# Optimization experiments

Hardware: AMD Instinct MI355X
Metric: run time of the kernel (lower is better)

## Reference

```python
import jax, jax.numpy as jnp
import numpy as np
import math

D_MODEL = 1024
N_HEAD = 16
D_HEAD = D_MODEL // N_HEAD


def setup_inputs() -> dict:
    key = jax.random.key(0)
    k0, k1, k2, k3, k4 = jax.random.split(key, 5)
    B, N = 4, 2048
    inp = jax.random.normal(k0, (B, N, D_MODEL), dtype=jnp.float32)
    # causal mask: True = keep (masked_fill on ~mask)
    mask = jnp.tril(jnp.ones((N, N), dtype=bool))
    # qkv_proj Linear(d_model, 3*d_model); output Linear(d_model, d_model)
    s_in = 1.0 / math.sqrt(D_MODEL)
    W_qkv = jax.random.uniform(k1, (D_MODEL, 3 * D_MODEL), jnp.float32, -s_in, s_in)
    b_qkv = jax.random.uniform(k2, (3 * D_MODEL,), jnp.float32, -s_in, s_in)
    W_out = jax.random.uniform(k3, (D_MODEL, D_MODEL), jnp.float32, -s_in, s_in)
    b_out = jax.random.uniform(k4, (D_MODEL,), jnp.float32, -s_in, s_in)
    return {"input": inp, "W_qkv": W_qkv, "b_qkv": b_qkv,
            "W_out": W_out, "b_out": b_out, "mask": mask}


def reference(input, W_qkv, b_qkv, W_out, b_out, mask):
    B, N, d = input.shape
    qkv = input @ W_qkv + b_qkv                       # [B,N,3d]  (dropout=eval no-op)
    q, k, v = jnp.split(qkv, 3, axis=-1)
    # [B,N,H,Dh] -> [B,H,N,Dh]
    q = q.reshape(B, N, N_HEAD, D_HEAD).transpose(0, 2, 1, 3)
    k = k.reshape(B, N, N_HEAD, D_HEAD).transpose(0, 2, 1, 3)
    v = v.reshape(B, N, N_HEAD, D_HEAD).transpose(0, 2, 1, 3)
    scale = 1.0 / math.sqrt(D_HEAD)
    scores = jnp.einsum('bhqd,bhkd->bhqk', q, k) * scale   # [B,H,N,N]
    scores = jnp.where(mask, scores, -jnp.inf)
    attn = jax.nn.softmax(scores, axis=-1)
    out = jnp.einsum('bhqk,bhkd->bhqd', attn, v)           # [B,H,N,Dh]
    out = out.transpose(0, 2, 1, 3).reshape(B, N, d)       # concat heads
    return out @ W_out + b_out
```

## Files before the change

### kernel.cpp

```cpp
#include <hip/hip_runtime.h>
#include <hip/hip_bf16.h>

typedef unsigned short u16;
typedef unsigned u32;
typedef __attribute__((ext_vector_type(4))) unsigned short u16x4;
typedef __attribute__((ext_vector_type(8))) unsigned short u16x8;
typedef __attribute__((ext_vector_type(4))) unsigned u32x4;
typedef __attribute__((ext_vector_type(8))) __bf16 bf16x8;
typedef __attribute__((ext_vector_type(4))) float f32x4;

typedef __attribute__((address_space(1))) void as1v;
typedef __attribute__((address_space(3))) void as3v;

#define MFMA16(a, b, c) __builtin_amdgcn_mfma_f32_16x16x32_bf16(a, b, c, 0, 0, 0)

#if __has_builtin(__builtin_amdgcn_permlane16_swap) && __has_builtin(__builtin_amdgcn_permlane32_swap)
#define HAVE_PERMLANE_SWAP 1
#else
#define HAVE_PERMLANE_SWAP 0
#endif

__device__ __forceinline__ u16 f2bf(float f) {
    unsigned u = __builtin_bit_cast(unsigned, f);
    u += 0x7fffu + ((u >> 16) & 1u);
    return (u16)(u >> 16);
}

__device__ __forceinline__ u32 pkbf(float lo, float hi) {
    u32 r;
    asm("v_cvt_pk_bf16_f32 %0, %1, %2" : "=v"(r) : "v"(lo), "v"(hi));
    return r;
}

__device__ __forceinline__ void gload16(const void* g, void* l) {
    __builtin_amdgcn_global_load_lds((as1v*)g, (as3v*)l, 16, 0, 0);
}

__device__ __forceinline__ float redmax_cross(float v) {
#if HAVE_PERMLANE_SWAP
    u32 xu = __builtin_bit_cast(u32, v);
    auto r16 = __builtin_amdgcn_permlane16_swap(xu, xu, false, false);
    float a = fmaxf(__builtin_bit_cast(float, (u32)r16[0]),
                    __builtin_bit_cast(float, (u32)r16[1]));
    u32 au = __builtin_bit_cast(u32, a);
    auto r32 = __builtin_amdgcn_permlane32_swap(au, au, false, false);
    return fmaxf(__builtin_bit_cast(float, (u32)r32[0]),
                 __builtin_bit_cast(float, (u32)r32[1]));
#else
    v = fmaxf(v, __shfl_xor(v, 16, 64));
    return fmaxf(v, __shfl_xor(v, 32, 64));
#endif
}

__device__ __forceinline__ float redsum_cross(float v) {
#if HAVE_PERMLANE_SWAP
    u32 xu = __builtin_bit_cast(u32, v);
    auto r16 = __builtin_amdgcn_permlane16_swap(xu, xu, false, false);
    float a = __builtin_bit_cast(float, (u32)r16[0]) +
              __builtin_bit_cast(float, (u32)r16[1]);
    u32 au = __builtin_bit_cast(u32, a);
    auto r32 = __builtin_amdgcn_permlane32_swap(au, au, false, false);
    return __builtin_bit_cast(float, (u32)r32[0]) +
           __builtin_bit_cast(float, (u32)r32[1]);
#else
    v += __shfl_xor(v, 16, 64);
    return v + __shfl_xor(v, 32, 64);
#endif
}

__global__ void convert_f32_bf16(const float* __restrict__ in, u16* __restrict__ out, int n4) {
    int i = blockIdx.x * blockDim.x + threadIdx.x;
    if (i < n4) {
        float4 v = *(const float4*)&in[(size_t)i * 4];
        u16x4 o;
        o.x = f2bf(v.x); o.y = f2bf(v.y); o.z = f2bf(v.z); o.w = f2bf(v.w);
        *(u16x4*)&out[(size_t)i * 4] = o;
    }
}

__global__ void transpose_convert(const float* __restrict__ in, u16* __restrict__ out, int R, int C) {
    __shared__ float tl[64][65];
    const int rb = blockIdx.x, cb = blockIdx.y;
    const int tid = threadIdx.x;
    for (int it = 0; it < 4; ++it) {
        int lin = (tid + it * 256) * 4;
        int r = lin >> 6, c = lin & 63;
        float4 v = *(const float4*)&in[(size_t)(rb * 64 + r) * C + cb * 64 + c];
        tl[r][c + 0] = v.x; tl[r][c + 1] = v.y; tl[r][c + 2] = v.z; tl[r][c + 3] = v.w;
    }
    __syncthreads();
    for (int it = 0; it < 4; ++it) {
        int lin = (tid + it * 256) * 4;
        int oc = lin >> 6, orr = lin & 63;
        u16x4 o;
        o.x = f2bf(tl[orr + 0][oc]);
        o.y = f2bf(tl[orr + 1][oc]);
        o.z = f2bf(tl[orr + 2][oc]);
        o.w = f2bf(tl[orr + 3][oc]);
        *(u16x4*)&out[(size_t)(cb * 64 + oc) * R + rb * 64 + orr] = o;
    }
}

__global__ __launch_bounds__(256, 3) void gemm128_qkv(
    const u16* __restrict__ A, const u16* __restrict__ Bt, const float* __restrict__ bias,
    u16* __restrict__ qb, u16* __restrict__ kb, u16* __restrict__ vtb) {
    constexpr int K = 1024;
    constexpr int NT = 32;
    __shared__ u16 ldsu[24576];

    const int bid = blockIdx.x;
    const int s = (bid & 7) * 192 + (bid >> 3);
    const int bm = s / 24, bn = s % 24;

    const int tid = threadIdx.x, wid = tid >> 6, lane = tid & 63;
    const int wr = wid >> 1, wc = wid & 1;
    const int l15 = lane & 15, lhi = lane >> 4;

    const int sslot = (lane & 7) ^ (lane >> 3);
    const int kcol = (sslot & 3) * 8;
    const int mloc = (lane >> 3) * 2 + (sslot >> 2);

    const u16* Arow[2];
    const u16* Brow[2];
#pragma unroll
    for (int li = 0; li < 2; ++li) {
        int sg = wid * 2 + li;
        Arow[li] = A + (size_t)(bm * 128 + sg * 16 + mloc) * K + kcol;
        Brow[li] = Bt + (size_t)(bn * 128 + sg * 16 + mloc) * K + kcol;
    }

    auto stageA = [&](int buf, int t) {
#pragma unroll
        for (int li = 0; li < 2; ++li) {
            int sg = wid * 2 + li;
            gload16(Arow[li] + t * 32, (char*)ldsu + buf * 16384 + sg * 1024);
        }
    };
    auto stageB = [&](int buf, int t) {
#pragma unroll
        for (int li = 0; li < 2; ++li) {
            int sg = wid * 2 + li;
            gload16(Brow[li] + t * 32, (char*)ldsu + buf * 16384 + 8192 + sg * 1024);
        }
    };

    const int rslot = ((l15 & 1) * 4 + lhi) ^ ((l15 >> 1) & 7);
    const int fragoff = (l15 >> 1) * 64 + rslot * 8;

    f32x4 acc[4][4];
#pragma unroll
    for (int i = 0; i < 4; ++i)
#pragma unroll
        for (int j = 0; j < 4; ++j) acc[i][j] = (f32x4){0.f, 0.f, 0.f, 0.f};

    auto doTile = [&](int cur, int tstage, bool dostage) {
        const u16* Ab = ldsu + cur * 8192 + wr * 2048 + fragoff;
        const u16* Bb = ldsu + cur * 8192 + 4096 + wc * 2048 + fragoff;
        bf16x8 af[4], b0, b1;
#pragma unroll
        for (int mf = 0; mf < 4; ++mf) af[mf] = *(const bf16x8*)(Ab + mf * 512);
        b0 = *(const bf16x8*)(Bb);
        b1 = *(const bf16x8*)(Bb + 512);
        if (dostage) stageA((tstage * 43691) >> 17  == -1 ? 0 : tstage % 3, tstage);
        __builtin_amdgcn_s_setprio(1);
#pragma unroll
        for (int mf = 0; mf < 4; ++mf) {
            acc[mf][0] = MFMA16(af[mf], b0, acc[mf][0]);
            acc[mf][1] = MFMA16(af[mf], b1, acc[mf][1]);
        }
        __builtin_amdgcn_s_setprio(0);
        b0 = *(const bf16x8*)(Bb + 1024);
        b1 = *(const bf16x8*)(Bb + 1536);
        if (dostage) stageB(tstage % 3, tstage);
        __builtin_amdgcn_s_setprio(1);
#pragma unroll
        for (int mf = 0; mf < 4; ++mf) {
            acc[mf][2] = MFMA16(af[mf], b0, acc[mf][2]);
            acc[mf][3] = MFMA16(af[mf], b1, acc[mf][3]);
        }
        __builtin_amdgcn_s_setprio(0);
    };

    stageA(0, 0); stageB(0, 0);
    stageA(1, 1); stageB(1, 1);
    asm volatile("s_waitcnt vmcnt(4)" ::: "memory");
    __builtin_amdgcn_s_barrier();
    __builtin_amdgcn_sched_barrier(0);

    for (int t = 0; t < NT - 2; ++t) {
        doTile(t % 3, t + 2, true);
        asm volatile("s_waitcnt vmcnt(4)" ::: "memory");
        __builtin_amdgcn_s_barrier();
        __builtin_amdgcn_sched_barrier(0);
    }
    doTile((NT - 2) % 3, 0, false);
    asm volatile("s_waitcnt vmcnt(0)" ::: "memory");
    __builtin_amdgcn_s_barrier();
    __builtin_amdgcn_sched_barrier(0);
    doTile((NT - 1) % 3, 0, false);

    const int cg0 = bn * 128 + wc * 64;
    const int which = cg0 >> 10, rem = cg0 & 1023;
    const int hh = rem >> 6, dh0 = rem & 63;
    const int rgb0 = bm * 128 + wr * 64;
    const int bb = rgb0 >> 11, n0 = rgb0 & 2047;

    if (which == 2) {
        const size_t vbase = ((size_t)(bb * 16 + hh) * 64 + dh0) * 2048 + (size_t)n0;
#pragma unroll
        for (int nt = 0; nt < 4; ++nt) {
            float bv = bias[cg0 + nt * 16 + l15];
            size_t rowb = vbase + (size_t)(nt * 16 + l15) * 2048;
#pragma unroll
            for (int mt = 0; mt < 4; ++mt) {
                u16x4 w;
#pragma unroll
                for (int v = 0; v < 4; ++v) w[v] = f2bf(acc[mt][nt][v] + bv);
                *(u16x4*)&vtb[rowb + mt * 16 + lhi * 4] = w;
            }
        }
    } else {
        u16* dst = (which == 0) ? qb : kb;
        const float qs = (which == 0) ? 0.18033688011112042f : 1.0f;
        const size_t gbase = (((size_t)bb * 16 + hh) * 2048 + n0) * 64 + dh0;
#pragma unroll
        for (int nt = 0; nt < 4; ++nt) {
            float bv = bias[cg0 + nt * 16 + l15];
#pragma unroll
            for (int mt = 0; mt < 4; ++mt)
#pragma unroll
                for (int v = 0; v < 4; ++v) {
                    int n = mt * 16 + lhi * 4 + v;
                    dst[gbase + (size_t)n * 64 + nt * 16 + l15] =
                        f2bf((acc[mt][nt][v] + bv) * qs);
                }
        }
    }
}

__global__ __launch_bounds__(512, 2) void gemm256_out(
    const u16* __restrict__ A, const u16* __restrict__ Bt, const float* __restrict__ bias,
    float* __restrict__ outf) {
    constexpr int K = 1024;
    constexpr int NT = 32;
    __shared__ u16 ldsu[49152];

    const int bid = blockIdx.x;
    const int swz = (bid & 7) * 32 + (bid >> 3);
    const int bm = swz >> 3, bn = swz & 7;

    const int tid = threadIdx.x, wid = tid >> 6, lane = tid & 63;
    const int wr = wid >> 2, wc = wid & 3;
    const int l15 = lane & 15, lhi = lane >> 4;

    const int sslot = (lane & 7) ^ (lane >> 3);
    const int kcol = (sslot & 3) * 8;
    const int mloc = (lane >> 3) * 2 + (sslot >> 2);

    const u16* Arow[2];
#pragma unroll
    for (int li = 0; li < 2; ++li) {
        int sg = wid * 2 + li;
        Arow[li] = A + (size_t)(bm * 256 + sg * 16 + mloc) * K + kcol;
    }
    const u16* Brow = Bt + (size_t)(bn * 128 + wid * 16 + mloc) * K + kcol;

    auto stageA = [&](int buf, int t) {
#pragma unroll
        for (int li = 0; li < 2; ++li) {
            int sg = wid * 2 + li;
            gload16(Arow[li] + t * 32, (char*)ldsu + buf * 24576 + sg * 1024);
        }
    };
    auto stageB = [&](int buf, int t) {
        gload16(Brow + t * 32, (char*)ldsu + buf * 24576 + 16384 + wid * 1024);
    };

    const int rslot = ((l15 & 1) * 4 + lhi) ^ ((l15 >> 1) & 7);
    const int fragoff = (l15 >> 1) * 64 + rslot * 8;

    f32x4 acc[8][2];
#pragma unroll
    for (int i = 0; i < 8; ++i) {
        acc[i][0] = (f32x4){0.f, 0.f, 0.f, 0.f};
        acc[i][1] = (f32x4){0.f, 0.f, 0.f, 0.f};
    }

    auto doTile = [&](int cur, int tstage, bool dostage) {
        const u16* Ab = ldsu + cur * 12288 + wr * 4096 + fragoff;
        const u16* Bb = ldsu + cur * 12288 + 8192 + wc * 1024 + fragoff;
        bf16x8 af[8], b0, b1;
#pragma unroll
        for (int mf = 0; mf < 8; ++mf) af[mf] = *(const bf16x8*)(Ab + mf * 512);
        b0 = *(const bf16x8*)(Bb);
        b1 = *(const bf16x8*)(Bb + 512);
        if (dostage) stageA(tstage & 3, tstage);
        __builtin_amdgcn_s_setprio(1);
#pragma unroll
        for (int mf = 0; mf < 8; ++mf) acc[mf][0] = MFMA16(af[mf], b0, acc[mf][0]);
        __builtin_amdgcn_s_setprio(0);
        if (dostage) stageB(tstage & 3, tstage);
        __builtin_amdgcn_s_setprio(1);
#pragma unroll
        for (int mf = 0; mf < 8; ++mf) acc[mf][1] = MFMA16(af[mf], b1, acc[mf][1]);
        __builtin_amdgcn_s_setprio(0);
    };

    stageA(0, 0); stageB(0, 0);
    stageA(1, 1); stageB(1, 1);
    stageA(2, 2); stageB(2, 2);
    asm volatile("s_waitcnt vmcnt(6)" ::: "memory");
    __builtin_amdgcn_s_barrier();
    __builtin_amdgcn_sched_barrier(0);

    for (int t = 0; t < NT - 3; ++t) {
        doTile(t & 3, t + 3, true);
        asm volatile("s_waitcnt vmcnt(6)" ::: "memory");
        __builtin_amdgcn_s_barrier();
        __builtin_amdgcn_sched_barrier(0);
    }
    doTile((NT - 3) & 3, 0, false);
    asm volatile("s_waitcnt vmcnt(3)" ::: "memory");
    __builtin_amdgcn_s_barrier();
    __builtin_amdgcn_sched_barrier(0);
    doTile((NT - 2) & 3, 0, false);
    asm volatile("s_waitcnt vmcnt(0)" ::: "memory");
    __builtin_amdgcn_s_barrier();
    __builtin_amdgcn_sched_barrier(0);
    doTile((NT - 1) & 3, 0, false);

#pragma unroll
    for (int nf = 0; nf < 2; ++nf) {
        int cg = bn * 128 + wc * 32 + nf * 16 + l15;
        float bv = bias[cg];
#pragma unroll
        for (int mf = 0; mf < 8; ++mf) {
            int rgb = bm * 256 + wr * 128 + mf * 16 + lhi * 4;
#pragma unroll
            for (int v = 0; v < 4; ++v)
                outf[(size_t)(rgb + v) * 1024 + cg] = acc[mf][nf][v] + bv;
        }
    }
}

__global__ __launch_bounds__(256, 4) void attn_kernel(
    const u16* __restrict__ qbuf, const u16* __restrict__ kbuf,
    const u16* __restrict__ vtb, u16* __restrict__ obuf) {
    __shared__ u16 Kl[2][64 * 64];
    __shared__ u16 Vl[2][64 * 64];
    const int bid = blockIdx.x;
    const int rr = bid >> 8;
    const int pp = (bid >> 6) & 3;
    const int c = (rr & 1) ? (((rr >> 1) << 2) + pp)
                           : (15 - ((rr >> 1) << 2) - pp);
    const int bh = ((bid & 7) << 3) + ((bid >> 3) & 7);
    const int b = bh >> 4, h = bh & 15;
    const int tid = threadIdx.x, wid = tid >> 6, lane = tid & 63;
    const int l15 = lane & 15, lhi = lane >> 4;
    const int q0 = c * 128 + wid * 32;
    const int ntW = 2 * c + (wid >> 1) + 1;
    const int ntmax = 2 * c + 2;

    auto loadQ = [&](int qbase, bf16x8* dst) {
        const u16* qp = qbuf + ((size_t)bh * 2048 + qbase + l15) * 64 + lhi * 8;
        dst[0] = *(const bf16x8*)(qp);
        dst[1] = *(const bf16x8*)(qp + 32);
    };
    bf16x8 qf0[2], qf1[2];
    loadQ(q0, qf0); loadQ(q0 + 16, qf1);

    float m0 = -1e30f, l0 = 0.f, m1 = -1e30f, l1 = 0.f;
    f32x4 o0[4], o1[4];
#pragma unroll
    for (int d = 0; d < 4; ++d) {
        o0[d] = (f32x4){0.f, 0.f, 0.f, 0.f};
        o1[d] = (f32x4){0.f, 0.f, 0.f, 0.f};
    }

    const int srow = lane >> 3;
    const int scolb = ((lane & 7) * 16) ^ (srow << 4);

    auto stage = [&](int buf, int t) {
        const int kbase = t * 64;
#pragma unroll
        for (int s = 0; s < 2; ++s) {
            int sg = wid * 2 + s;
            int row = sg * 8 + srow;
            const u16* gk = kbuf + ((size_t)bh * 2048 + kbase + row) * 64 + (scolb >> 1);
            gload16(gk, (char*)Kl[buf] + sg * 1024);
            const u16* gv = vtb + ((size_t)bh * 64 + row) * 2048 + kbase + (scolb >> 1);
            gload16(gv, (char*)Vl[buf] + sg * 1024);
        }
    };

    auto smax = [&](f32x4* s, int qg0, int t, float& m, float& l, f32x4* oa, u32* pw) {
        const int qg = qg0 + l15;
        if (64 * t + 63 > qg0) {
#pragma unroll
            for (int kb4 = 0; kb4 < 4; ++kb4)
#pragma unroll
                for (int v = 0; v < 4; ++v) {
                    int kg = 64 * t + kb4 * 16 + lhi * 4 + v;
                    if (kg > qg) s[kb4][v] = -1e30f;
                }
        }
        float pm = fmaxf(fmaxf(fmaxf(s[0][0], s[0][1]), fmaxf(s[0][2], s[0][3])),
                         fmaxf(fmaxf(s[1][0], s[1][1]), fmaxf(s[1][2], s[1][3])));
        pm = fmaxf(pm, fmaxf(fmaxf(fmaxf(s[2][0], s[2][1]), fmaxf(s[2][2], s[2][3])),
                             fmaxf(fmaxf(s[3][0], s[3][1]), fmaxf(s[3][2], s[3][3]))));
        pm = redmax_cross(pm);
        if (!__all(pm <= m + 8.f)) {
            float nm = fmaxf(m, pm);
            float f = exp2f(m - nm);
            m = nm;
            l *= f;
#pragma unroll
            for (int d = 0; d < 4; ++d)
#pragma unroll
                for (int v = 0; v < 4; ++v) oa[d][v] *= f;
        }
        float rs = 0.f;
#pragma unroll
        for (int kb4 = 0; kb4 < 4; ++kb4)
#pragma unroll
            for (int v = 0; v < 4; ++v) {
                float e = exp2f(s[kb4][v] - m);
                s[kb4][v] = e;
                rs += e;
            }
        l += redsum_cross(rs);
        pw[0] = pkbf(s[0][0], s[0][1]); pw[1] = pkbf(s[0][2], s[0][3]);
        pw[2] = pkbf(s[1][0], s[1][1]); pw[3] = pkbf(s[1][2], s[1][3]);
        pw[4] = pkbf(s[2][0], s[2][1]); pw[5] = pkbf(s[2][2], s[2][3]);
        pw[6] = pkbf(s[3][0], s[3][1]); pw[7] = pkbf(s[3][2], s[3][3]);
    };

    auto computeChunk = [&](const char* Kb, const char* Vb, int t) {
        f32x4 s0[4], s1[4];
        __builtin_amdgcn_s_setprio(1);
#pragma unroll
        for (int kb4 = 0; kb4 < 4; ++kb4) {
            const int r = kb4 * 16 + l15;
            const int sw = (r & 7) << 4;
            const int rowb = r * 128;
            bf16x8 kf0 = *(const bf16x8*)(Kb + rowb + ((lhi * 16) ^ sw));
            bf16x8 kf1 = *(const bf16x8*)(Kb + rowb + ((64 + lhi * 16) ^ sw));
            f32x4 a0 = (f32x4){0.f, 0.f, 0.f, 0.f};
            a0 = MFMA16(kf0, qf0[0], a0);
            a0 = MFMA16(kf1, qf0[1], a0);
            s0[kb4] = a0;
            f32x4 a1 = (f32x4){0.f, 0.f, 0.f, 0.f};
            a1 = MFMA16(kf0, qf1[0], a1);
            a1 = MFMA16(kf1, qf1[1], a1);
            s1[kb4] = a1;
        }
        __builtin_amdgcn_s_setprio(0);
        u32 pw0[8], pw1[8];
        smax(s0, q0, t, m0, l0, o0, pw0);
        smax(s1, q0 + 16, t, m1, l1, o1, pw1);
        __builtin_amdgcn_s_setprio(1);
#pragma unroll
        for (int ks = 0; ks < 2; ++ks) {
            bf16x8 pb0 = __builtin_bit_cast(bf16x8,
                (u32x4){pw0[ks * 4 + 0], pw0[ks * 4 + 1], pw0[ks * 4 + 2], pw0[ks * 4 + 3]});
            bf16x8 pb1 = __builtin_bit_cast(bf16x8,
                (u32x4){pw1[ks * 4 + 0], pw1[ks * 4 + 1], pw1[ks * 4 + 2], pw1[ks * 4 + 3]});
#pragma unroll
            for (int dhb = 0; dhb < 4; ++dhb) {
                const int r = dhb * 16 + l15;
                const int sw = (r & 7) << 4;
                u16x4 v0 = *(const u16x4*)(Vb + r * 128 + ((ks * 64 + 8 * lhi) ^ sw));
                u16x4 v1 = *(const u16x4*)(Vb + r * 128 + ((ks * 64 + 32 + 8 * lhi) ^ sw));
                u16x8 vv = {v0[0], v0[1], v0[2], v0[3], v1[0], v1[1], v1[2], v1[3]};
                bf16x8 vf = __builtin_bit_cast(bf16x8, vv);
                o0[dhb] = MFMA16(vf, pb0, o0[dhb]);
                o1[dhb] = MFMA16(vf, pb1, o1[dhb]);
            }
        }
        __builtin_amdgcn_s_setprio(0);
    };

    stage(0, 0);
    int t = 0;
    for (;;) {
        __syncthreads();
        if (t + 1 < ntmax) stage(1, t + 1);
        if (t < ntW) computeChunk((const char*)Kl[0], (const char*)Vl[0], t);
        if (++t == ntmax) break;
        __syncthreads();
        if (t + 1 < ntmax) stage(0, t + 1);
        if (t < ntW) computeChunk((const char*)Kl[1], (const char*)Vl[1], t);
        if (++t == ntmax) break;
    }

    auto epi = [&](int qg0, float l, const f32x4* oa) {
        const float rl = 1.f / l;
        const int q = qg0 + l15;
        const size_t rowoff = ((size_t)b * 2048 + q) * 1024 + h * 64;
#pragma unroll
        for (int dhb = 0; dhb < 4; ++dhb) {
            u16x4 w;
#pragma unroll
            for (int v = 0; v < 4; ++v) w[v] = f2bf(oa[dhb][v] * rl);
            *(u16x4*)&obuf[rowoff + dhb * 16 + lhi * 4] = w;
        }
    };
    epi(q0, l0, o0);
    epi(q0 + 16, l1, o1);
}

extern "C" void kernel_launch(void* const* d_in, const int* in_sizes, int n_in,
                              void* d_out, int out_size, void* d_ws, size_t ws_size,
                              hipStream_t stream) {
    const float* inp   = (const float*)d_in[0];
    const float* W_qkv = (const float*)d_in[1];
    const float* b_qkv = (const float*)d_in[2];
    const float* W_out = (const float*)d_in[3];
    const float* b_out = (const float*)d_in[4];
    float* out = (float*)d_out;

    u16* xb   = (u16*)d_ws;
    u16* wqt  = xb + 8388608;
    u16* wot  = wqt + 3145728;
    u16* qbuf = wot + 1048576;
    u16* kbuf = qbuf + 8388608;
    u16* vtb  = kbuf + 8388608;
    u16* obuf = vtb + 8388608;

    convert_f32_bf16<<<8192, 256, 0, stream>>>(inp, xb, 2097152);
    transpose_convert<<<dim3(16, 48), 256, 0, stream>>>(W_qkv, wqt, 1024, 3072);
    transpose_convert<<<dim3(16, 16), 256, 0, stream>>>(W_out, wot, 1024, 1024);
    gemm128_qkv<<<1536, 256, 0, stream>>>(xb, wqt, b_qkv, qbuf, kbuf, vtb);
    attn_kernel<<<1024, 256, 0, stream>>>(qbuf, kbuf, vtb, obuf);
    gemm256_out<<<256, 512, 0, stream>>>(obuf, wot, b_out, out);
}
```

Baseline: 178.2 us.

## Split causal attention rows across blocks with log-sum-exp merge for balance

Each block pair now handles query chunk p fully plus half the key range of chunk 15-p, while the partner block does the other half. Partial outputs and their max/sum statistics are written out, and a new merge kernel combines them with log-sum-exp rescaling. The goal is equal work per block under the causal mask, replacing the earlier interleaved block ordering. The cost is an extra kernel launch, fp32 partial-output traffic through reused workspace, and a bf16 round trip on one of the two partials. It also simplifies a no-op expression in the GEMM stage index.

Measured after the change: 214.1 us. 1.2x slower.

```diff
diff --git a/kernel.cpp b/kernel.cpp
--- a/kernel.cpp
+++ b/kernel.cpp
@@ -24,6 +24,11 @@
     unsigned u = __builtin_bit_cast(unsigned, f);
     u += 0x7fffu + ((u >> 16) & 1u);
     return (u16)(u >> 16);
+}
+
+__device__ __forceinline__ float bf2f(u16 v) {
+    u32 u = ((u32)v) << 16;
+    return __builtin_bit_cast(float, u);
 }
 
 __device__ __forceinline__ u32 pkbf(float lo, float hi) {
@@ -161,7 +166,7 @@
         for (int mf = 0; mf < 4; ++mf) af[mf] = *(const bf16x8*)(Ab + mf * 512);
         b0 = *(const bf16x8*)(Bb);
         b1 = *(const bf16x8*)(Bb + 512);
-        if (dostage) stageA((tstage * 43691) >> 17  == -1 ? 0 : tstage % 3, tstage);
+        if (dostage) stageA(tstage % 3, tstage);
         __builtin_amdgcn_s_setprio(1);
 #pragma unroll
         for (int mf = 0; mf < 4; ++mf) {
@@ -345,37 +350,17 @@
 
 __global__ __launch_bounds__(256, 4) void attn_kernel(
     const u16* __restrict__ qbuf, const u16* __restrict__ kbuf,
-    const u16* __restrict__ vtb, u16* __restrict__ obuf) {
+    const u16* __restrict__ vtb, u16* __restrict__ obuf,
+    float* __restrict__ pbufA, float* __restrict__ mlbuf) {
     __shared__ u16 Kl[2][64 * 64];
     __shared__ u16 Vl[2][64 * 64];
     const int bid = blockIdx.x;
-    const int rr = bid >> 8;
-    const int pp = (bid >> 6) & 3;
-    const int c = (rr & 1) ? (((rr >> 1) << 2) + pp)
-                           : (15 - ((rr >> 1) << 2) - pp);
-    const int bh = ((bid & 7) << 3) + ((bid >> 3) & 7);
+    const int half = bid & 1;
+    const int p = (bid >> 1) & 7;
+    const int bh = bid >> 4;
     const int b = bh >> 4, h = bh & 15;
     const int tid = threadIdx.x, wid = tid >> 6, lane = tid & 63;
     const int l15 = lane & 15, lhi = lane >> 4;
-    const int q0 = c * 128 + wid * 32;
-    const int ntW = 2 * c + (wid >> 1) + 1;
-    const int ntmax = 2 * c + 2;
-
-    auto loadQ = [&](int qbase, bf16x8* dst) {
-        const u16* qp = qbuf + ((size_t)bh * 2048 + qbase + l15) * 64 + lhi * 8;
-        dst[0] = *(const bf16x8*)(qp);
-        dst[1] = *(const bf16x8*)(qp + 32);
-    };
-    bf16x8 qf0[2], qf1[2];
-    loadQ(q0, qf0); loadQ(q0 + 16, qf1);
-
-    float m0 = -1e30f, l0 = 0.f, m1 = -1e30f, l1 = 0.f;
-    f32x4 o0[4], o1[4];
-#pragma unroll
-    for (int d = 0; d < 4; ++d) {
-        o0[d] = (f32x4){0.f, 0.f, 0.f, 0.f};
-        o1[d] = (f32x4){0.f, 0.f, 0.f, 0.f};
-    }
 
     const int srow = lane >> 3;
     const int scolb = ((lane & 7) * 16) ^ (srow << 4);
@@ -393,120 +378,205 @@
         }
     };
 
-    auto smax = [&](f32x4* s, int qg0, int t, float& m, float& l, f32x4* oa, u32* pw) {
-        const int qg = qg0 + l15;
-        if (64 * t + 63 > qg0) {
+    auto run_piece = [&](int c, int t0, int t1, int mode) {
+        const int q0 = c * 128 + wid * 32;
+        bf16x8 qf0[2], qf1[2];
+        {
+            const u16* qp0 = qbuf + ((size_t)bh * 2048 + q0 + l15) * 64 + lhi * 8;
+            const u16* qp1 = qbuf + ((size_t)bh * 2048 + q0 + 16 + l15) * 64 + lhi * 8;
+            qf0[0] = *(const bf16x8*)(qp0); qf0[1] = *(const bf16x8*)(qp0 + 32);
+            qf1[0] = *(const bf16x8*)(qp1); qf1[1] = *(const bf16x8*)(qp1 + 32);
+        }
+        float m0 = -1e30f, l0 = 0.f, m1 = -1e30f, l1 = 0.f;
+        f32x4 o0[4], o1[4];
+#pragma unroll
+        for (int d = 0; d < 4; ++d) {
+            o0[d] = (f32x4){0.f, 0.f, 0.f, 0.f};
+            o1[d] = (f32x4){0.f, 0.f, 0.f, 0.f};
+        }
+        const int ntW = 2 * c + (wid >> 1) + 1;
+
+        auto smax = [&](f32x4* s, int qg0, int t, float& m, float& l, f32x4* oa, u32* pw) {
+            const int qg = qg0 + l15;
+            if (64 * t + 63 > qg0) {
+#pragma unroll
+                for (int kb4 = 0; kb4 < 4; ++kb4)
+#pragma unroll
+                    for (int v = 0; v < 4; ++v) {
+                        int kg = 64 * t + kb4 * 16 + lhi * 4 + v;
+                        if (kg > qg) s[kb4][v] = -1e30f;
+                    }
+            }
+            float pm = fmaxf(fmaxf(fmaxf(s[0][0], s[0][1]), fmaxf(s[0][2], s[0][3])),
+                             fmaxf(fmaxf(s[1][0], s[1][1]), fmaxf(s[1][2], s[1][3])));
+            pm = fmaxf(pm, fmaxf(fmaxf(fmaxf(s[2][0], s[2][1]), fmaxf(s[2][2], s[2][3])),
+                                 fmaxf(fmaxf(s[3][0], s[3][1]), fmaxf(s[3][2], s[3][3]))));
+            pm = redmax_cross(pm);
+            if (!__all(pm <= m + 8.f)) {
+                float nm = fmaxf(m, pm);
+                float f = exp2f(m - nm);
+                m = nm;
+                l *= f;
+#pragma unroll
+                for (int d = 0; d < 4; ++d)
+#pragma unroll
+                    for (int v = 0; v < 4; ++v) oa[d][v] *= f;
+            }
+            float rs = 0.f;
 #pragma unroll
             for (int kb4 = 0; kb4 < 4; ++kb4)
 #pragma unroll
                 for (int v = 0; v < 4; ++v) {
-                    int kg = 64 * t + kb4 * 16 + lhi * 4 + v;
-                    if (kg > qg) s[kb4][v] = -1e30f;
+                    float e = exp2f(s[kb4][v] - m);
+                    s[kb4][v] = e;
+                    rs += e;
                 }
-        }
-        float pm = fmaxf(fmaxf(fmaxf(s[0][0], s[0][1]), fmaxf(s[0][2], s[0][3])),
-                         fmaxf(fmaxf(s[1][0], s[1][1]), fmaxf(s[1][2], s[1][3])));
-        pm = fmaxf(pm, fmaxf(fmaxf(fmaxf(s[2][0], s[2][1]), fmaxf(s[2][2], s[2][3])),
-                             fmaxf(fmaxf(s[3][0], s[3][1]), fmaxf(s[3][2], s[3][3]))));
-        pm = redmax_cross(pm);
-        if (!__all(pm <= m + 8.f)) {
-            float nm = fmaxf(m, pm);
-            float f = exp2f(m - nm);
-            m = nm;
-            l *= f;
-#pragma unroll
-            for (int d = 0; d < 4; ++d)
-#pragma unroll
-                for (int v = 0; v < 4; ++v) oa[d][v] *= f;
-        }
-        float rs = 0.f;
-#pragma unroll
-        for (int kb4 = 0; kb4 < 4; ++kb4)
-#pragma unroll
-            for (int v = 0; v < 4; ++v) {
-                float e = exp2f(s[kb4][v] - m);
-                s[kb4][v] = e;
-                rs += e;
+            l += redsum_cross(rs);
+            pw[0] = pkbf(s[0][0], s[0][1]); pw[1] = pkbf(s[0][2], s[0][3]);
+            pw[2] = pkbf(s[1][0], s[1][1]); pw[3] = pkbf(s[1][2], s[1][3]);
+            pw[4] = pkbf(s[2][0], s[2][1]); pw[5] = pkbf(s[2][2], s[2][3]);
+            pw[6] = pkbf(s[3][0], s[3][1]); pw[7] = pkbf(s[3][2], s[3][3]);
+        };
+
+        auto computeChunk = [&](const char* Kb, const char* Vb, int t) {
+            f32x4 s0[4], s1[4];
+            __builtin_amdgcn_s_setprio(1);
+#pragma unroll
+            for (int kb4 = 0; kb4 < 4; ++kb4) {
+                const int r = kb4 * 16 + l15;
+                const int sw = (r & 7) << 4;
+                const int rowb = r * 128;
+                bf16x8 kf0 = *(const bf16x8*)(Kb + rowb + ((lhi * 16) ^ sw));
+                bf16x8 kf1 = *(const bf16x8*)(Kb + rowb + ((64 + lhi * 16) ^ sw));
+                f32x4 a0 = (f32x4){0.f, 0.f, 0.f, 0.f};
+                a0 = MFMA16(kf0, qf0[0], a0);
+                a0 = MFMA16(kf1, qf0[1], a0);
+                s0[kb4] = a0;
+                f32x4 a1 = (f32x4){0.f, 0.f, 0.f, 0.f};
+                a1 = MFMA16(kf0, qf1[0], a1);
+                a1 = MFMA16(kf1, qf1[1], a1);
+                s1[kb4] = a1;
             }
-        l += redsum_cross(rs);
-        pw[0] = pkbf(s[0][0], s[0][1]); pw[1] = pkbf(s[0][2], s[0][3]);
-        pw[2] = pkbf(s[1][0], s[1][1]); pw[3] = pkbf(s[1][2], s[1][3]);
-        pw[4] = pkbf(s[2][0], s[2][1]); pw[5] = pkbf(s[2][2], s[2][3]);
-        pw[6] = pkbf(s[3][0], s[3][1]); pw[7] = pkbf(s[3][2], s[3][3]);
-    };
-
-    auto computeChunk = [&](const char* Kb, const char* Vb, int t) {
-        f32x4 s0[4], s1[4];
-        __builtin_amdgcn_s_setprio(1);
-#pragma unroll
-        for (int kb4 = 0; kb4 < 4; ++kb4) {
-            const int r = kb4 * 16 + l15;
-            const int sw = (r & 7) << 4;
-            const int rowb = r * 128;
-            bf16x8 kf0 = *(const bf16x8*)(Kb + rowb + ((lhi * 16) ^ sw));
-            bf16x8 kf1 = *(const bf16x8*)(Kb + rowb + ((64 + lhi * 16) ^ sw));
-            f32x4 a0 = (f32x4){0.f, 0.f, 0.f, 0.f};
-            a0 = MFMA16(kf0, qf0[0], a0);
-            a0 = MFMA16(kf1, qf0[1], a0);
-            s0[kb4] = a0;
-            f32x4 a1 = (f32x4){0.f, 0.f, 0.f, 0.f};
-            a1 = MFMA16(kf0, qf1[0], a1);
-            a1 = MFMA16(kf1, qf1[1], a1);
-            s1[kb4] = a1;
-        }
-        __builtin_amdgcn_s_setprio(0);
-        u32 pw0[8], pw1[8];
-        smax(s0, q0, t, m0, l0, o0, pw0);
-        smax(s1, q0 + 16, t, m1, l1, o1, pw1);
-        __builtin_amdgcn_s_setprio(1);
-#pragma unroll
-        for (int ks = 0; ks < 2; ++ks) {
-            bf16x8 pb0 = __builtin_bit_cast(bf16x8,
-                (u32x4){pw0[ks * 4 + 0], pw0[ks * 4 + 1], pw0[ks * 4 + 2], pw0[ks * 4 + 3]});
-            bf16x8 pb1 = __builtin_bit_cast(bf16x8,
-                (u32x4){pw1[ks * 4 + 0], pw1[ks * 4 + 1], pw1[ks * 4 + 2], pw1[ks * 4 + 3]});
-#pragma unroll
-            for (int dhb = 0; dhb < 4; ++dhb) {
-                const int r = dhb * 16 + l15;
-                const int sw = (r & 7) << 4;
-                u16x4 v0 = *(const u16x4*)(Vb + r * 128 + ((ks * 64 + 8 * lhi) ^ sw));
-                u16x4 v1 = *(const u16x4*)(Vb + r * 128 + ((ks * 64 + 32 + 8 * lhi) ^ sw));
-                u16x8 vv = {v0[0], v0[1], v0[2], v0[3], v1[0], v1[1], v1[2], v1[3]};
-                bf16x8 vf = __builtin_bit_cast(bf16x8, vv);
-                o0[dhb] = MFMA16(vf, pb0, o0[dhb]);
-                o1[dhb] = MFMA16(vf, pb1, o1[dhb]);
+            __builtin_amdgcn_s_setprio(0);
+            u32 pw0[8], pw1[8];
+            smax(s0, q0, t, m0, l0, o0, pw0);
+            smax(s1, q0 + 16, t, m1, l1, o1, pw1);
+            __builtin_amdgcn_s_setprio(1);
+#pragma unroll
+            for (int ks = 0; ks < 2; ++ks) {
+                bf16x8 pb0 = __builtin_bit_cast(bf16x8,
+                    (u32x4){pw0[ks * 4 + 0], pw0[ks * 4 + 1], pw0[ks * 4 + 2], pw0[ks * 4 + 3]});
+                bf16x8 pb1 = __builtin_bit_cast(bf16x8,
+                    (u32x4){pw1[ks * 4 + 0], pw1[ks * 4 + 1], pw1[ks * 4 + 2], pw1[ks * 4 + 3]});
+#pragma unroll
+                for (int dhb = 0; dhb < 4; ++dhb) {
+                    const int r = dhb * 16 + l15;
+                    const int sw = (r & 7) << 4;
+                    u16x4 v0 = *(const u16x4*)(Vb + r * 128 + ((ks * 64 + 8 * lhi) ^ sw));
+                    u16x4 v1 = *(const u16x4*)(Vb + r * 128 + ((ks * 64 + 32 + 8 * lhi) ^ sw));
+                    u16x8 vv = {v0[0], v0[1], v0[2], v0[3], v1[0], v1[1], v1[2], v1[3]};
+                    bf16x8 vf = __builtin_bit_cast(bf16x8, vv);
+                    o0[dhb] = MFMA16(vf, pb0, o0[dhb]);
+                    o1[dhb] = MFMA16(vf, pb1, o1[dhb]);
+                }
             }
-        }
-        __builtin_amdgcn_s_setprio(0);
-    };
-
-    stage(0, 0);
-    int t = 0;
-    for (;;) {
+            __builtin_amdgcn_s_setprio(0);
+        };
+
         __syncthreads();
-        if (t + 1 < ntmax) stage(1, t + 1);
-        if (t < ntW) computeChunk((const char*)Kl[0], (const char*)Vl[0], t);
-        if (++t == ntmax) break;
-        __syncthreads();
-        if (t + 1 < ntmax) stage(0, t + 1);
-        if (t < ntW) computeChunk((const char*)Kl[1], (const char*)Vl[1], t);
-        if (++t == ntmax) break;
-    }
-
-    auto epi = [&](int qg0, float l, const f32x4* oa) {
-        const float rl = 1.f / l;
-        const int q = qg0 + l15;
-        const size_t rowoff = ((size_t)b * 2048 + q) * 1024 + h * 64;
-#pragma unroll
-        for (int dhb = 0; dhb < 4; ++dhb) {
-            u16x4 w;
-#pragma unroll
-            for (int v = 0; v < 4; ++v) w[v] = f2bf(oa[dhb][v] * rl);
-            *(u16x4*)&obuf[rowoff + dhb * 16 + lhi * 4] = w;
-        }
-    };
-    epi(q0, l0, o0);
-    epi(q0 + 16, l1, o1);
+        stage(0, t0);
+        int t = t0;
+        for (;;) {
+            __syncthreads();
+            if (t + 1 < t1) stage(((t - t0) & 1) ^ 1, t + 1);
+            if (t < ntW) computeChunk((const char*)Kl[(t - t0) & 1],
+                                      (const char*)Vl[(t - t0) & 1], t);
+            if (++t == t1) break;
+        }
+
+        const int pi = 15 - c;
+        if (mode == 0) {
+            auto epi = [&](int goff, float l, const f32x4* oa) {
+                const float rl = 1.f / l;
+                const int q = q0 + goff + l15;
+                const size_t rowoff = ((size_t)b * 2048 + q) * 1024 + h * 64;
+#pragma unroll
+                for (int dhb = 0; dhb < 4; ++dhb) {
+                    u16x4 w;
+#pragma unroll
+                    for (int v = 0; v < 4; ++v) w[v] = f2bf(oa[dhb][v] * rl);
+                    *(u16x4*)&obuf[rowoff + dhb * 16 + lhi * 4] = w;
+                }
+            };
+            epi(0, l0, o0);
+            epi(16, l1, o1);
+        } else if (mode == 1) {
+            auto epi = [&](int goff, float m, float l, const f32x4* oa) {
+                const int ql = wid * 32 + goff + l15;
+                const size_t rowi = ((size_t)bh * 8 + pi) * 128 + ql;
+                float* prow = pbufA + rowi * 64;
+#pragma unroll
+                for (int dhb = 0; dhb < 4; ++dhb)
+                    *(f32x4*)&prow[dhb * 16 + lhi * 4] = oa[dhb];
+                if (lhi == 0) { mlbuf[rowi] = m; mlbuf[65536 + rowi] = l; }
+            };
+            epi(0, m0, l0, o0);
+            epi(16, m1, l1, o1);
+        } else {
+            auto epi = [&](int goff, float m, float l, const f32x4* oa) {
+                const float rl = 1.f / l;
+                const int q = q0 + goff + l15;
+                const size_t rowoff = ((size_t)b * 2048 + q) * 1024 + h * 64;
+#pragma unroll
+                for (int dhb = 0; dhb < 4; ++dhb) {
+                    u16x4 w;
+#pragma unroll
+                    for (int v = 0; v < 4; ++v) w[v] = f2bf(oa[dhb][v] * rl);
+                    *(u16x4*)&obuf[rowoff + dhb * 16 + lhi * 4] = w;
+                }
+                const int ql = wid * 32 + goff + l15;
+                const size_t rowi = ((size_t)bh * 8 + pi) * 128 + ql;
+                if (lhi == 0) { mlbuf[131072 + rowi] = m; mlbuf[196608 + rowi] = l; }
+            };
+            epi(0, m0, l0, o0);
+            epi(16, m1, l1, o1);
+        }
+    };
+
+    if (half == 0) {
+        run_piece(p, 0, 2 * p + 2, 0);
+        run_piece(15 - p, 0, 15 - 2 * p, 1);
+    } else {
+        run_piece(15 - p, 15 - 2 * p, 32 - 2 * p, 2);
+    }
+}
+
+__global__ __launch_bounds__(256) void merge_lse(
+    const float* __restrict__ pbufA, const float* __restrict__ mlbuf,
+    u16* __restrict__ obuf) {
+    const int gid = blockIdx.x * 256 + threadIdx.x;
+    const int rid = gid >> 2, seg = gid & 3;
+    const float m1 = mlbuf[rid], l1 = mlbuf[65536 + rid];
+    const float m2 = mlbuf[131072 + rid], l2 = mlbuf[196608 + rid];
+    const float M = fmaxf(m1, m2);
+    const float f1 = exp2f(m1 - M), f2 = exp2f(m2 - M);
+    const float rden = 1.f / (l1 * f1 + l2 * f2);
+    const float w2 = l2 * f2;
+    const int bh = rid >> 10, rem = rid & 1023, pp = rem >> 7, ql = rem & 127;
+    const int b = bh >> 4, h = bh & 15;
+    const int qg = (15 - pp) * 128 + ql;
+    u16* orow = obuf + ((size_t)b * 2048 + qg) * 1024 + h * 64 + seg * 16;
+    const float* prow = pbufA + (size_t)rid * 64 + seg * 16;
+#pragma unroll
+    for (int j = 0; j < 4; ++j) {
+        f32x4 o1 = *(const f32x4*)&prow[j * 4];
+        u16x4 o2 = *(const u16x4*)&orow[j * 4];
+        u16x4 w;
+#pragma unroll
+        for (int v = 0; v < 4; ++v)
+            w[v] = f2bf((o1[v] * f1 + bf2f(o2[v]) * w2) * rden);
+        *(u16x4*)&orow[j * 4] = w;
+    }
 }
 
 extern "C" void kernel_launch(void* const* d_in, const int* in_sizes, int n_in,
@@ -526,11 +596,14 @@
     u16* kbuf = qbuf + 8388608;
     u16* vtb  = kbuf + 8388608;
     u16* obuf = vtb + 8388608;
+    float* pbufA = (float*)xb;
+    float* mlbuf = (float*)wqt;
 
     convert_f32_bf16<<<8192, 256, 0, stream>>>(inp, xb, 2097152);
     transpose_convert<<<dim3(16, 48), 256, 0, stream>>>(W_qkv, wqt, 1024, 3072);
     transpose_convert<<<dim3(16, 16), 256, 0, stream>>>(W_out, wot, 1024, 1024);
     gemm128_qkv<<<1536, 256, 0, stream>>>(xb, wqt, b_qkv, qbuf, kbuf, vtb);
-    attn_kernel<<<1024, 256, 0, stream>>>(qbuf, kbuf, vtb, obuf);
+    attn_kernel<<<1024, 256, 0, stream>>>(qbuf, kbuf, vtb, obuf, pbufA, mlbuf);
+    merge_lse<<<1024, 256, 0, stream>>>(pbufA, mlbuf, obuf);
     gemm256_out<<<256, 512, 0, stream>>>(obuf, wot, b_out, out);
 }
```

## Replace 256x128 output GEMM with 128x128 tiles and triple-buffered pipeline

Applied to the files above, without the earlier changes.

The output projection GEMM moves from 256x128 tiles with 512 threads and a 4-stage buffer to 128x128 tiles with 256 threads and a 3-stage buffer, which doubles the grid to 512 blocks. This reuses the QKV GEMM's tile structure, so the kernel uses less LDS and can fit more blocks per CU, and more blocks spread across the CUs. In exchange each block gets less operand reuse and one fewer prefetch stage. A no-op expression in the QKV stageA buffer index is also simplified.

Result: no change. 179.2 us (median of 2 runs) (+0.6%).

```diff
diff --git a/kernel.cpp b/kernel.cpp
--- a/kernel.cpp
+++ b/kernel.cpp
@@ -161,7 +161,7 @@
         for (int mf = 0; mf < 4; ++mf) af[mf] = *(const bf16x8*)(Ab + mf * 512);
         b0 = *(const bf16x8*)(Bb);
         b1 = *(const bf16x8*)(Bb + 512);
-        if (dostage) stageA((tstage * 43691) >> 17  == -1 ? 0 : tstage % 3, tstage);
+        if (dostage) stageA(tstage % 3, tstage);
         __builtin_amdgcn_s_setprio(1);
 #pragma unroll
         for (int mf = 0; mf < 4; ++mf) {
@@ -238,19 +238,19 @@
     }
 }
 
-__global__ __launch_bounds__(512, 2) void gemm256_out(
+__global__ __launch_bounds__(256, 3) void gemm128_out(
     const u16* __restrict__ A, const u16* __restrict__ Bt, const float* __restrict__ bias,
     float* __restrict__ outf) {
     constexpr int K = 1024;
     constexpr int NT = 32;
-    __shared__ u16 ldsu[49152];
+    __shared__ u16 ldsu[24576];
 
     const int bid = blockIdx.x;
-    const int swz = (bid & 7) * 32 + (bid >> 3);
-    const int bm = swz >> 3, bn = swz & 7;
+    const int s = (bid & 7) * 64 + (bid >> 3);
+    const int bm = s >> 3, bn = s & 7;
 
     const int tid = threadIdx.x, wid = tid >> 6, lane = tid & 63;
-    const int wr = wid >> 2, wc = wid & 3;
+    const int wr = wid >> 1, wc = wid & 1;
     const int l15 = lane & 15, lhi = lane >> 4;
 
     const int sslot = (lane & 7) ^ (lane >> 3);
@@ -258,87 +258,94 @@
     const int mloc = (lane >> 3) * 2 + (sslot >> 2);
 
     const u16* Arow[2];
+    const u16* Brow[2];
 #pragma unroll
     for (int li = 0; li < 2; ++li) {
         int sg = wid * 2 + li;
-        Arow[li] = A + (size_t)(bm * 256 + sg * 16 + mloc) * K + kcol;
-    }
-    const u16* Brow = Bt + (size_t)(bn * 128 + wid * 16 + mloc) * K + kcol;
+        Arow[li] = A + (size_t)(bm * 128 + sg * 16 + mloc) * K + kcol;
+        Brow[li] = Bt + (size_t)(bn * 128 + sg * 16 + mloc) * K + kcol;
+    }
 
     auto stageA = [&](int buf, int t) {
 #pragma unroll
         for (int li = 0; li < 2; ++li) {
             int sg = wid * 2 + li;
-            gload16(Arow[li] + t * 32, (char*)ldsu + buf * 24576 + sg * 1024);
+            gload16(Arow[li] + t * 32, (char*)ldsu + buf * 16384 + sg * 1024);
         }
     };
     auto stageB = [&](int buf, int t) {
-        gload16(Brow + t * 32, (char*)ldsu + buf * 24576 + 16384 + wid * 1024);
+#pragma unroll
+        for (int li = 0; li < 2; ++li) {
+            int sg = wid * 2 + li;
+            gload16(Brow[li] + t * 32, (char*)ldsu + buf * 16384 + 8192 + sg * 1024);
+        }
     };
 
     const int rslot = ((l15 & 1) * 4 + lhi) ^ ((l15 >> 1) & 7);
     const int fragoff = (l15 >> 1) * 64 + rslot * 8;
 
-    f32x4 acc[8][2];
-#pragma unroll
-    for (int i = 0; i < 8; ++i) {
-        acc[i][0] = (f32x4){0.f, 0.f, 0.f, 0.f};
-        acc[i][1] = (f32x4){0.f, 0.f, 0.f, 0.f};
-    }
+    f32x4 acc[4][4];
+#pragma unroll
+    for (int i = 0; i < 4; ++i)
+#pragma unroll
+        for (int j = 0; j < 4; ++j) acc[i][j] = (f32x4){0.f, 0.f, 0.f, 0.f};
 
     auto doTile = [&](int cur, int tstage, bool dostage) {
-        const u16* Ab = ldsu + cur * 12288 + wr * 4096 + fragoff;
-        const u16* Bb = ldsu + cur * 12288 + 8192 + wc * 1024 + fragoff;
-        bf16x8 af[8], b0, b1;
-#pragma unroll
-        for (int mf = 0; mf < 8; ++mf) af[mf] = *(const bf16x8*)(Ab + mf * 512);
+        const u16* Ab = ldsu + cur * 8192 + wr * 2048 + fragoff;
+        const u16* Bb = ldsu + cur * 8192 + 4096 + wc * 2048 + fragoff;
+        bf16x8 af[4], b0, b1;
+#pragma unroll
+        for (int mf = 0; mf < 4; ++mf) af[mf] = *(const bf16x8*)(Ab + mf * 512);
         b0 = *(const bf16x8*)(Bb);
         b1 = *(const bf16x8*)(Bb + 512);
-        if (dostage) stageA(tstage & 3, tstage);
+        if (dostage) stageA(tstage % 3, tstage);
         __builtin_amdgcn_s_setprio(1);
 #pragma unroll
-        for (int mf = 0; mf < 8; ++mf) acc[mf][0] = MFMA16(af[mf], b0, acc[mf][0]);
+        for (int mf = 0; mf < 4; ++mf) {
+            acc[mf][0] = MFMA16(af[mf], b0, acc[mf][0]);
+            acc[mf][1] = MFMA16(af[mf], b1, acc[mf][1]);
+        }
         __builtin_amdgcn_s_setprio(0);
-        if (dostage) stageB(tstage & 3, tstage);
+        b0 = *(const bf16x8*)(Bb + 1024);
+        b1 = *(const bf16x8*)(Bb + 1536);
+        if (dostage) stageB(tstage % 3, tstage);
         __builtin_amdgcn_s_setprio(1);
 #pragma unroll
-        for (int mf = 0; mf < 8; ++mf) acc[mf][1] = MFMA16(af[mf], b1, acc[mf][1]);
+        for (int mf = 0; mf < 4; ++mf) {
+            acc[mf][2] = MFMA16(af[mf], b0, acc[mf][2]);
+            acc[mf][3] = MFMA16(af[mf], b1, acc[mf][3]);
+        }
         __builtin_amdgcn_s_setprio(0);
     };
 
     stageA(0, 0); stageB(0, 0);
     stageA(1, 1); stageB(1, 1);
-    stageA(2, 2); stageB(2, 2);
-    asm volatile("s_waitcnt vmcnt(6)" ::: "memory");
+    asm volatile("s_waitcnt vmcnt(4)" ::: "memory");
     __builtin_amdgcn_s_barrier();
     __builtin_amdgcn_sched_barrier(0);
 
-    for (int t = 0; t < NT - 3; ++t) {
-        doTile(t & 3, t + 3, true);
-        asm volatile("s_waitcnt vmcnt(6)" ::: "memory");
+    for (int t = 0; t < NT - 2; ++t) {
+        doTile(t % 3, t + 2, true);
+        asm volatile("s_waitcnt vmcnt(4)" ::: "memory");
         __builtin_amdgcn_s_barrier();
         __builtin_amdgcn_sched_barrier(0);
     }
-    doTile((NT - 3) & 3, 0, false);
-    asm volatile("s_waitcnt vmcnt(3)" ::: "memory");
-    __builtin_amdgcn_s_barrier();
-    __builtin_amdgcn_sched_barrier(0);
-    doTile((NT - 2) & 3, 0, false);
+    doTile((NT - 2) % 3, 0, false);
     asm volatile("s_waitcnt vmcnt(0)" ::: "memory");
     __builtin_amdgcn_s_barrier();
     __builtin_amdgcn_sched_barrier(0);
-    doTile((NT - 1) & 3, 0, false);
-
-#pragma unroll
-    for (int nf = 0; nf < 2; ++nf) {
-        int cg = bn * 128 + wc * 32 + nf * 16 + l15;
+    doTile((NT - 1) % 3, 0, false);
+
+#pragma unroll
+    for (int nt = 0; nt < 4; ++nt) {
+        int cg = bn * 128 + wc * 64 + nt * 16 + l15;
         float bv = bias[cg];
 #pragma unroll
-        for (int mf = 0; mf < 8; ++mf) {
-            int rgb = bm * 256 + wr * 128 + mf * 16 + lhi * 4;
+        for (int mt = 0; mt < 4; ++mt) {
+            int rg = bm * 128 + wr * 64 + mt * 16 + lhi * 4;
 #pragma unroll
             for (int v = 0; v < 4; ++v)
-                outf[(size_t)(rgb + v) * 1024 + cg] = acc[mf][nf][v] + bv;
+                outf[(size_t)(rg + v) * 1024 + cg] = acc[mt][nt][v] + bv;
         }
     }
 }
@@ -532,5 +539,5 @@
     transpose_convert<<<dim3(16, 16), 256, 0, stream>>>(W_out, wot, 1024, 1024);
     gemm128_qkv<<<1536, 256, 0, stream>>>(xb, wqt, b_qkv, qbuf, kbuf, vtb);
     attn_kernel<<<1024, 256, 0, stream>>>(qbuf, kbuf, vtb, obuf);
-    gemm256_out<<<256, 512, 0, stream>>>(obuf, wot, b_out, out);
-}
+    gemm128_out<<<512, 256, 0, stream>>>(obuf, wot, b_out, out);
+}
```
